# Kernel optimization log

Measured on AMD Instinct MI355X. Metric: run time of the kernel, lower is better.

Reference implementation:

```python
import jax, jax.numpy as jnp
import numpy as np

M = 100000
K = 27            # (2*radius+1)^3, radius=1
D = 64            # attn_dim
C_GEO = 64
C_SEM = 96
NUM_CLASSES = 13
RADIUS = 1
DIAM = 3
EPS = 1e-5


def setup_inputs() -> dict:
    key = jax.random.key(0)
    ks = jax.random.split(key, 16)
    geo_feat_M = jax.random.normal(ks[0], (M, C_GEO), jnp.float32)
    sem_feat_M = jax.random.normal(ks[1], (M, C_SEM), jnp.float32)
    coords = jax.random.randint(ks[2], (M, 3), 0, 64, jnp.int32)
    neighbor_idx = jax.random.randint(ks[3], (M, K), 0, M, jnp.int64)
    # KNN always returns self as a neighbor -> guarantee at least one valid entry
    neighbor_idx = neighbor_idx.at[:, 0].set(jnp.arange(M, dtype=jnp.int64))
    s = 0.05
    return {
        "geo_feat_M": geo_feat_M,
        "sem_feat_M": sem_feat_M,
        "coords": coords,
        "neighbor_idx": neighbor_idx,
        "W_geo": jax.random.normal(ks[4], (C_GEO, D), jnp.float32) * s,
        "gamma": jnp.ones((D,), jnp.float32),
        "beta": jnp.zeros((D,), jnp.float32),
        "W_bdy": jax.random.normal(ks[5], (D, 1), jnp.float32) * s,
        "b_bdy": jnp.zeros((1,), jnp.float32),
        "W_q": jax.random.normal(ks[6], (D, D), jnp.float32) * s,
        "W_k": jax.random.normal(ks[7], (D, D), jnp.float32) * s,
        "W_v": jax.random.normal(ks[8], (C_SEM, D), jnp.float32) * s,
        "pos_emb": jax.random.normal(ks[9], (DIAM ** 3, D), jnp.float32) * s,
        "W_out": jax.random.normal(ks[10], (D, D), jnp.float32) * s,
        "b_out": jnp.zeros((D,), jnp.float32),
        "W_cls": jax.random.normal(ks[11], (D, NUM_CLASSES), jnp.float32) * s,
        "b_cls": jnp.zeros((NUM_CLASSES,), jnp.float32),
    }


def _layernorm(x, gamma, beta):
    mu = jnp.mean(x, axis=-1, keepdims=True)
    var = jnp.mean(jnp.square(x - mu), axis=-1, keepdims=True)
    return (x - mu) * jax.lax.rsqrt(var + EPS) * gamma + beta


def reference(geo_feat_M, sem_feat_M, coords, neighbor_idx,
              W_geo, gamma, beta, W_bdy, b_bdy, W_q, W_k, W_v,
              pos_emb, W_out, b_out, W_cls, b_cls):
    # geometry branch
    Q_geo = jax.nn.relu(_layernorm(geo_feat_M @ W_geo, gamma, beta))  # [M, D]
    bdy_logits = Q_geo @ W_bdy + b_bdy                                # [M, 1]

    # neighbor geometry: valid mask + relative-position embedding index
    nbr_coords = coords[neighbor_idx]                                 # [M, K, 3]
    rel = nbr_coords - coords[:, None, :]                             # [M, K, 3]
    valid_mask = jnp.max(jnp.abs(rel).astype(jnp.float32), axis=-1) <= RADIUS + 0.1
    rel_int = jnp.clip(rel + RADIUS, 0, 2 * RADIUS)
    pos_indices = rel_int[:, :, 0] * DIAM ** 2 + rel_int[:, :, 1] * DIAM + rel_int[:, :, 2]

    # gather neighbor features
    K_feat = Q_geo[neighbor_idx]                                      # [M, K, D]
    V_feat = sem_feat_M[neighbor_idx]                                 # [M, K, C_SEM]

    Qp = Q_geo @ W_q                                                  # [M, D]
    Kp = K_feat @ W_k + pos_emb[pos_indices]                          # [M, K, D]
    Vp = V_feat @ W_v                                                 # [M, K, D]

    attn_logits = jnp.einsum("md,mkd->mk", Qp, Kp) / jnp.sqrt(jnp.float32(D))
    attn_logits = jnp.where(valid_mask, attn_logits, jnp.float32(-10000.0))
    affinity = jax.nn.softmax(attn_logits, axis=-1)                   # [M, K]

    refined = jnp.einsum("mk,mkd->md", affinity, Vp) + sem_feat_M @ W_v
    refined_feat = refined @ W_out + b_out                            # [M, D]
    logits = refined_feat @ W_cls + b_cls                             # [M, 13]
    return (logits, bdy_logits, affinity[:, None, :], refined_feat, neighbor_idx, valid_mask)
```

## Files before the change

kernel.cpp:

```cpp
#include <hip/hip_runtime.h>
#include <hip/hip_bf16.h>

#define M_PTS 100000
#define KN 27
#define CS 96
#define NC 13

#define OFF_LOGITS 0ull
#define OFF_BDY    1300000ull
#define OFF_AFF    1400000ull
#define OFF_RF     4100000ull
#define OFF_NBR    10500000ull
#define OFF_MASK   13200000ull

#define WS_QG   0ull
#define WS_U    6400000ull
#define WS_P    12800000ull
#define WS_WGEO 15500000ull
#define WS_WQK  (WS_WGEO + 4608ull)
#define WS_WPOS (WS_WQK + 4608ull)
#define WS_W1   (WS_WPOS + 2304ull)
#define WS_W2   (WS_W1 + 6656ull)
#define WS_B2   (WS_W2 + 1664ull)
#define WS_VM   (WS_B2 + 32ull)

typedef float f4 __attribute__((ext_vector_type(4)));
typedef float f32x4 __attribute__((ext_vector_type(4)));
typedef short bf16x8 __attribute__((ext_vector_type(8)));
typedef short s16x4 __attribute__((ext_vector_type(4)));

__device__ __forceinline__ short f2bf(float f) {
  union { float f; unsigned int u; } x; x.f = f;
  unsigned int r = x.u + 0x7fffu + ((x.u >> 16) & 1u);
  return (short)(r >> 16);
}
__device__ __forceinline__ float bf2f(unsigned short u) {
  union { unsigned int i; float f; } x; x.i = ((unsigned int)u) << 16;
  return x.f;
}
__device__ __forceinline__ bool nbr_is64(const void* nbrv) {
  const int* w = (const int*)nbrv;
  bool is64 = true;
#pragma unroll
  for (int j = 1; j < 64; j += 2) is64 = is64 && (w[j] == 0);
  return is64;
}
__device__ __forceinline__ long long nbr_at(const void* nbrv, bool is64, size_t i) {
  return is64 ? ((const long long*)nbrv)[i] : (long long)((const int*)nbrv)[i];
}

__global__ __launch_bounds__(256) void k0(const float* __restrict__ Wgeo,
                                          const float* __restrict__ Wbdy,
                                          const float* __restrict__ Wq,
                                          const float* __restrict__ Wk,
                                          const float* __restrict__ Wv,
                                          const float* __restrict__ pos,
                                          const float* __restrict__ Wout,
                                          const float* __restrict__ bout,
                                          const float* __restrict__ Wcls,
                                          const float* __restrict__ bcls,
                                          short* __restrict__ ws) {
  __shared__ float V[64 * NC];
  const int tid = threadIdx.x, blk = blockIdx.x;
  if (blk < 32) {
    for (int i = blk * 256 + tid; i < 16384; i += 8192) {
      if (i < 4096) {
        const int d = i >> 6, c = i & 63;
        ws[WS_WGEO + d * 72 + c] = f2bf(Wgeo[c * 64 + d]);
      } else if (i < 8192) {
        const int t = i - 4096, d = t >> 6, c = t & 63;
        float s = 0.f;
#pragma unroll 8
        for (int q = 0; q < 64; ++q) s = fmaf(Wq[c * 64 + q], Wk[d * 64 + q], s);
        ws[WS_WQK + d * 72 + c] = f2bf(s);
      } else if (i < 10240) {
        const int t = i - 8192, j = t >> 6, c = t & 63;
        float s = 0.f;
        if (j < 27) {
#pragma unroll 8
          for (int q = 0; q < 64; ++q) s = fmaf(Wq[c * 64 + q], pos[j * 64 + q], s);
        } else if (j == 27) {
          s = Wbdy[c];
        }
        ws[WS_WPOS + j * 72 + c] = f2bf(s);
      } else {
        const int t = i - 10240, d = t / 96, sc = t % 96;
        float a = 0.f;
#pragma unroll 8
        for (int q = 0; q < 64; ++q) a = fmaf(Wv[sc * 64 + q], Wout[q * 64 + d], a);
        ws[WS_W1 + d * 104 + sc] = f2bf(a);
      }
    }
  } else {
    for (int i = tid; i < 64 * NC; i += 256) {
      const int t = i / NC, j = i % NC;
      float a = 0.f;
#pragma unroll 8
      for (int d = 0; d < 64; ++d) a = fmaf(Wout[t * 64 + d], Wcls[d * NC + j], a);
      V[i] = a;
    }
    __syncthreads();
    const int g = (blk - 32) * 256 + tid;
    if (g < 16 * 96) {
      const int j = g / 96, s = g % 96;
      float a = 0.f;
      if (j < NC) {
#pragma unroll 8
        for (int t = 0; t < 64; ++t) a = fmaf(Wv[s * 64 + t], V[t * NC + j], a);
      }
      ws[WS_W2 + j * 104 + s] = f2bf(a);
    }
    if (blk == 32 && tid < 16) {
      float a = 0.f;
      if (tid < NC) {
        for (int d = 0; d < 64; ++d) a = fmaf(bout[d], Wcls[d * NC + tid], a);
        a += bcls[tid];
      }
      ((float*)(ws + WS_B2))[tid] = a;
    }
  }
}

__global__ __launch_bounds__(256) void k1(const float* __restrict__ geo,
                                          const int* __restrict__ coords,
                                          const void* __restrict__ nbrv,
                                          const float* __restrict__ gamma,
                                          const float* __restrict__ beta,
                                          const float* __restrict__ bbdy,
                                          const short* __restrict__ ws,
                                          short* __restrict__ Qg,
                                          short* __restrict__ U,
                                          short* __restrict__ P,
                                          unsigned int* __restrict__ vmask,
                                          float* __restrict__ out) {
  __shared__ short sX[4608];
  __shared__ short sQ[4608];
  __shared__ short sWg[4608];
  __shared__ short sWqk[4608];
  __shared__ short sWp[2304];
  const int tid = threadIdx.x;
  {
    const bf16x8* a = (const bf16x8*)(ws + WS_WGEO);
    const bf16x8* b = (const bf16x8*)(ws + WS_WQK);
    const bf16x8* c = (const bf16x8*)(ws + WS_WPOS);
    for (int i = tid; i < 576; i += 256) ((bf16x8*)sWg)[i] = a[i];
    for (int i = tid; i < 576; i += 256) ((bf16x8*)sWqk)[i] = b[i];
    for (int i = tid; i < 288; i += 256) ((bf16x8*)sWp)[i] = c[i];
  }
  const int m0 = blockIdx.x * 64;
  {
    const int r = tid >> 2, qq = tid & 3;
    const int m = min(m0 + r, M_PTS - 1);
    const f4* g = (const f4*)(geo + (size_t)m * 64 + qq * 16);
    const f4 a = g[0], b = g[1], c = g[2], d = g[3];
    bf16x8 lo, hi;
    lo[0]=f2bf(a.x); lo[1]=f2bf(a.y); lo[2]=f2bf(a.z); lo[3]=f2bf(a.w);
    lo[4]=f2bf(b.x); lo[5]=f2bf(b.y); lo[6]=f2bf(b.z); lo[7]=f2bf(b.w);
    hi[0]=f2bf(c.x); hi[1]=f2bf(c.y); hi[2]=f2bf(c.z); hi[3]=f2bf(c.w);
    hi[4]=f2bf(d.x); hi[5]=f2bf(d.y); hi[6]=f2bf(d.z); hi[7]=f2bf(d.w);
    *(bf16x8*)&sX[r * 72 + qq * 16] = lo;
    *(bf16x8*)&sX[r * 72 + qq * 16 + 8] = hi;
  }
  __syncthreads();

  const int lane = tid & 63, w = tid >> 6;
  const int hi4 = lane >> 4, lo16 = lane & 15;
  const int R = w * 16;

  f32x4 acc[4] = {};
#pragma unroll
  for (int kk = 0; kk < 2; ++kk) {
    const bf16x8 a = *(const bf16x8*)&sX[(R + lo16) * 72 + kk * 32 + hi4 * 8];
#pragma unroll
    for (int n = 0; n < 4; ++n) {
      const bf16x8 b = *(const bf16x8*)&sWg[(n * 16 + lo16) * 72 + kk * 32 + hi4 * 8];
      acc[n] = __builtin_amdgcn_mfma_f32_16x16x32_bf16(a, b, acc[n], 0, 0, 0);
    }
  }
  float gam4[4], bet4[4];
#pragma unroll
  for (int n = 0; n < 4; ++n) { gam4[n] = gamma[n * 16 + lo16]; bet4[n] = beta[n * 16 + lo16]; }
#pragma unroll
  for (int j = 0; j < 4; ++j) {
    float s = acc[0][j] + acc[1][j] + acc[2][j] + acc[3][j];
#pragma unroll
    for (int o = 1; o <= 8; o <<= 1) s += __shfl_xor(s, o, 64);
    const float mu = s * (1.f / 64.f);
    float vs = 0.f;
#pragma unroll
    for (int n = 0; n < 4; ++n) { const float d = acc[n][j] - mu; vs = fmaf(d, d, vs); }
#pragma unroll
    for (int o = 1; o <= 8; o <<= 1) vs += __shfl_xor(vs, o, 64);
    const float inv = rsqrtf(vs * (1.f / 64.f) + 1e-5f);
#pragma unroll
    for (int n = 0; n < 4; ++n) {
      const float q = fmaxf(fmaf((acc[n][j] - mu) * inv, gam4[n], bet4[n]), 0.f);
      sQ[(R + hi4 * 4 + j) * 72 + n * 16 + lo16] = f2bf(q);
    }
  }
  __syncthreads();
  f32x4 au[4] = {};
#pragma unroll
  for (int kk = 0; kk < 2; ++kk) {
    const bf16x8 a = *(const bf16x8*)&sQ[(R + lo16) * 72 + kk * 32 + hi4 * 8];
#pragma unroll
    for (int n = 0; n < 4; ++n) {
      const bf16x8 b = *(const bf16x8*)&sWqk[(n * 16 + lo16) * 72 + kk * 32 + hi4 * 8];
      au[n] = __builtin_amdgcn_mfma_f32_16x16x32_bf16(a, b, au[n], 0, 0, 0);
    }
  }
#pragma unroll
  for (int j = 0; j < 4; ++j)
#pragma unroll
    for (int n = 0; n < 4; ++n)
      sX[(R + hi4 * 4 + j) * 72 + n * 16 + lo16] = f2bf(au[n][j]);
  f32x4 ap[2] = {};
#pragma unroll
  for (int kk = 0; kk < 2; ++kk) {
    const bf16x8 a = *(const bf16x8*)&sQ[(R + lo16) * 72 + kk * 32 + hi4 * 8];
#pragma unroll
    for (int n = 0; n < 2; ++n) {
      const bf16x8 b = *(const bf16x8*)&sWp[(n * 16 + lo16) * 72 + kk * 32 + hi4 * 8];
      ap[n] = __builtin_amdgcn_mfma_f32_16x16x32_bf16(a, b, ap[n], 0, 0, 0);
    }
  }
  const float bb = bbdy[0];
#pragma unroll
  for (int n = 0; n < 2; ++n) {
    const int col = n * 16 + lo16;
#pragma unroll
    for (int j = 0; j < 4; ++j) {
      const int m = m0 + R + hi4 * 4 + j;
      if (m < M_PTS) {
        if (col < KN) P[(size_t)m * KN + col] = f2bf(ap[n][j]);
        else if (col == KN) out[OFF_BDY + m] = ap[n][j] + bb;
      }
    }
  }
  __syncthreads();
  for (int i = tid; i < 512; i += 256) {
    const int r = i >> 3, u = i & 7;
    const int m = m0 + r;
    if (m < M_PTS) {
      *(bf16x8*)&Qg[(size_t)m * 64 + u * 8] = *(const bf16x8*)&sQ[r * 72 + u * 8];
      *(bf16x8*)&U[(size_t)m * 64 + u * 8] = *(const bf16x8*)&sX[r * 72 + u * 8];
    }
  }
  {
    const bool is64 = nbr_is64(nbrv);
    const int r = tid >> 2, qq = tid & 3;
    const int m = m0 + r;
    unsigned vbits = 0;
    if (m < M_PTS) {
      const int c0 = coords[m * 3 + 0], c1 = coords[m * 3 + 1], c2 = coords[m * 3 + 2];
      const int kq0 = qq * 7;
      const int cnt = (qq == 3) ? 6 : 7;
#pragma unroll
      for (int t = 0; t < 7; ++t) {
        if (t < cnt) {
          const size_t ni = (size_t)m * KN + kq0 + t;
          const long long nk = nbr_at(nbrv, is64, ni);
          const int dx = coords[nk * 3 + 0] - c0;
          const int dy = coords[nk * 3 + 1] - c1;
          const int dz = coords[nk * 3 + 2] - c2;
          const int valid = (max(max(abs(dx), abs(dy)), abs(dz)) <= 1) ? 1 : 0;
          out[OFF_NBR + ni] = (float)nk;
          out[OFF_MASK + ni] = (float)valid;
          vbits |= (unsigned)valid << (kq0 + t);
        }
      }
    }
    vbits |= __shfl_xor(vbits, 1, 64);
    vbits |= __shfl_xor(vbits, 2, 64);
    if (qq == 0 && m < M_PTS) vmask[m] = vbits;
  }
}

__global__ __launch_bounds__(256) void k2(const float* __restrict__ sem,
                                          const int* __restrict__ coords,
                                          const void* __restrict__ nbrv,
                                          const float* __restrict__ bout,
                                          const short* __restrict__ ws,
                                          const short* __restrict__ Qg,
                                          const short* __restrict__ U,
                                          const short* __restrict__ P,
                                          const unsigned int* __restrict__ vmask,
                                          float* __restrict__ out) {
  __shared__ short sW1[6656];
  __shared__ short sW2[1664];
  __shared__ short sS[6656];
  const int tid = threadIdx.x;
  {
    const bf16x8* a = (const bf16x8*)(ws + WS_W1);
    const bf16x8* b = (const bf16x8*)(ws + WS_W2);
    for (int i = tid; i < 832; i += 256) ((bf16x8*)sW1)[i] = a[i];
    for (int i = tid; i < 208; i += 256) ((bf16x8*)sW2)[i] = b[i];
  }
  const float* b2 = (const float*)(ws + WS_B2);
  const bool is64 = nbr_is64(nbrv);
  __syncthreads();

  const int lane = tid & 63, w = tid >> 6;
  const int hi4 = lane >> 4, lo16 = lane & 15;
  const int R = w * 16;
  const int m0 = blockIdx.x * 64;
  const int pbase = m0 + R;
  const int l31 = lane & 31;
  const int nvr = max(0, min(16, M_PTS - pbase));

  unsigned mym = 0;
  if (lane < nvr) mym = vmask[pbase + lane];
  const unsigned long long cb = __ballot(__popc(mym) > 1);

  const int naff = nvr * KN;
#pragma unroll
  for (int it = 0; it < 7; ++it) {
    const int idx = it * 64 + lane;
    if (idx < naff) {
      const int p = idx / KN;
      if (!((cb >> p) & 1))
        out[OFF_AFF + (size_t)pbase * KN + idx] = (idx - p * KN == 0) ? 1.f : 0.f;
    }
  }
  {
    const f4* semb = (const f4*)(sem + (size_t)pbase * CS);
    const int nf4 = nvr * 24;
#pragma unroll
    for (int it = 0; it < 6; ++it) {
      const int idx = it * 64 + lane;
      if (idx < nf4) {
        const f4 v = semb[idx];
        const int linear = idx * 4, p = linear / 96, c = linear - p * 96;
        if (!((cb >> p) & 1)) {
          s16x4 st;
          st[0] = f2bf(2.f * v.x); st[1] = f2bf(2.f * v.y);
          st[2] = f2bf(2.f * v.z); st[3] = f2bf(2.f * v.w);
          *(s16x4*)&sS[(R + p) * 104 + c] = st;
        }
      }
    }
  }
  unsigned long long cbl = cb;
  while (cbl) {
    const int p = __ffsll(cbl) - 1; cbl &= cbl - 1;
    const int m = pbase + p;
    int nk = 0, vf = 0, pidx = 13;
    if (lane < KN) {
      nk = (int)nbr_at(nbrv, is64, (size_t)m * KN + lane);
      const int dx = coords[nk * 3 + 0] - coords[m * 3 + 0];
      const int dy = coords[nk * 3 + 1] - coords[m * 3 + 1];
      const int dz = coords[nk * 3 + 2] - coords[m * 3 + 2];
      vf = (max(max(abs(dx), abs(dy)), abs(dz)) <= 1) ? 1 : 0;
      pidx = vf ? ((dx + 1) * 9 + (dy + 1) * 3 + (dz + 1)) : 13;
    }
    const float pval = (lane < KN) ? bf2f((unsigned short)P[(size_t)m * KN + pidx]) : 0.f;
    const float uv = bf2f((unsigned short)U[(size_t)m * 64 + lane]);
    float lg = -10000.f;
    unsigned long long vb = __ballot(vf != 0);
    while (vb) {
      const int k = __ffsll(vb) - 1; vb &= vb - 1;
      const int nn = __shfl(nk, k, 64);
      float dd = bf2f((unsigned short)Qg[(size_t)nn * 64 + lane]) * uv;
#pragma unroll
      for (int o = 1; o < 64; o <<= 1) dd += __shfl_xor(dd, o, 64);
      const float pv = __shfl(pval, k, 64);
      if (lane == k) lg = (dd + pv) * 0.125f;
    }
    float mx = lg;
#pragma unroll
    for (int o = 1; o < 32; o <<= 1) mx = fmaxf(mx, __shfl_xor(mx, o, 64));
    const float e = (lane < KN) ? __expf(lg - mx) : 0.f;
    float ssum = e;
#pragma unroll
    for (int o = 1; o < 32; o <<= 1) ssum += __shfl_xor(ssum, o, 64);
    const float aa = e / ssum;
    if (lane < KN) out[OFF_AFF + (size_t)m * KN + lane] = aa;
    float slo = sem[(size_t)m * CS + lane];
    float shi = sem[(size_t)m * CS + 64 + l31];
    unsigned long long ab = __ballot(lane < KN && aa > 0.f);
    while (ab) {
      const int k = __ffsll(ab) - 1; ab &= ab - 1;
      const float ak = __shfl(aa, k, 64);
      const int nn = __shfl(nk, k, 64);
      slo = fmaf(ak, sem[(size_t)nn * CS + lane], slo);
      shi = fmaf(ak, sem[(size_t)nn * CS + 64 + l31], shi);
    }
    sS[(R + p) * 104 + lane] = f2bf(slo);
    if (lane < 32) sS[(R + p) * 104 + 64 + lane] = f2bf(shi);
  }
  __syncthreads();

  f32x4 ar[4] = {};
  f32x4 al = {};
#pragma unroll
  for (int kk = 0; kk < 3; ++kk) {
    const bf16x8 a = *(const bf16x8*)&sS[(R + lo16) * 104 + kk * 32 + hi4 * 8];
#pragma unroll
    for (int n = 0; n < 4; ++n) {
      const bf16x8 b = *(const bf16x8*)&sW1[(n * 16 + lo16) * 104 + kk * 32 + hi4 * 8];
      ar[n] = __builtin_amdgcn_mfma_f32_16x16x32_bf16(a, b, ar[n], 0, 0, 0);
    }
    const bf16x8 b = *(const bf16x8*)&sW2[lo16 * 104 + kk * 32 + hi4 * 8];
    al = __builtin_amdgcn_mfma_f32_16x16x32_bf16(a, b, al, 0, 0, 0);
  }
#pragma unroll
  for (int n = 0; n < 4; ++n) {
    const float bo = bout[n * 16 + lo16];
#pragma unroll
    for (int j = 0; j < 4; ++j) {
      const int m = m0 + R + hi4 * 4 + j;
      if (m < M_PTS) out[OFF_RF + (size_t)m * 64 + n * 16 + lo16] = ar[n][j] + bo;
    }
  }
  {
    const float bc = (lo16 < NC) ? b2[lo16] : 0.f;
#pragma unroll
    for (int j = 0; j < 4; ++j) {
      const int m = m0 + R + hi4 * 4 + j;
      if (m < M_PTS && lo16 < NC) out[OFF_LOGITS + (size_t)m * NC + lo16] = al[j] + bc;
    }
  }
}

extern "C" void kernel_launch(void* const* d_in, const int* in_sizes, int n_in,
                              void* d_out, int out_size, void* d_ws, size_t ws_size,
                              hipStream_t stream) {
  const float* geo = (const float*)d_in[0];
  const float* sem = (const float*)d_in[1];
  const int* coords = (const int*)d_in[2];
  const void* nbrv = (const void*)d_in[3];
  const float* Wgeo = (const float*)d_in[4];
  const float* gamma = (const float*)d_in[5];
  const float* beta = (const float*)d_in[6];
  const float* Wbdy = (const float*)d_in[7];
  const float* bbdy = (const float*)d_in[8];
  const float* Wq = (const float*)d_in[9];
  const float* Wk = (const float*)d_in[10];
  const float* Wv = (const float*)d_in[11];
  const float* pos = (const float*)d_in[12];
  const float* Wout = (const float*)d_in[13];
  const float* bout = (const float*)d_in[14];
  const float* Wcls = (const float*)d_in[15];
  const float* bcls = (const float*)d_in[16];

  short* ws = (short*)d_ws;
  short* Qg = ws + WS_QG;
  short* U = ws + WS_U;
  short* P = ws + WS_P;
  unsigned int* vmask = (unsigned int*)(ws + WS_VM);
  float* out = (float*)d_out;

  const int blocks = (M_PTS + 63) / 64;
  k0<<<38, 256, 0, stream>>>(Wgeo, Wbdy, Wq, Wk, Wv, pos, Wout, bout, Wcls, bcls, ws);
  k1<<<blocks, 256, 0, stream>>>(geo, coords, nbrv, gamma, beta, bbdy, ws, Qg, U, P, vmask, out);
  k2<<<blocks, 256, 0, stream>>>(sem, coords, nbrv, bout, ws, Qg, U, P, vmask, out);
}
```

Before: 222.7 us.

## Fuse simple-point path into k1 and process complex points in a compact persistent kernel

The common path (points with at most one valid neighbor) is now finished inside k1: it reuses shared memory to compute the sem-based refined features and logits with MFMA right after the geometry stage. U and P are written only for points with multiple valid neighbors. Those complex points are handled by a new persistent kernel k2r, launched on 128 blocks, which loops over tiles with one wave per tile and does the output projections with per-lane shuffle dot products instead of MFMA. This removes the full second pass over all points and the reload of vmask and weights in every tile, at the cost of a longer k1 with more shared memory and an unbalanced scalar tail for complex points.

```diff
diff --git a/kernel.cpp b/kernel.cpp
--- a/kernel.cpp
+++ b/kernel.cpp
@@ -5,6 +5,7 @@
 #define KN 27
 #define CS 96
 #define NC 13
+#define NTILES 1563
 
 #define OFF_LOGITS 0ull
 #define OFF_BDY    1300000ull
@@ -122,23 +123,32 @@
 }
 
 __global__ __launch_bounds__(256) void k1(const float* __restrict__ geo,
+                                          const float* __restrict__ sem,
                                           const int* __restrict__ coords,
                                           const void* __restrict__ nbrv,
                                           const float* __restrict__ gamma,
                                           const float* __restrict__ beta,
                                           const float* __restrict__ bbdy,
+                                          const float* __restrict__ bout,
                                           const short* __restrict__ ws,
                                           short* __restrict__ Qg,
                                           short* __restrict__ U,
                                           short* __restrict__ P,
                                           unsigned int* __restrict__ vmask,
                                           float* __restrict__ out) {
-  __shared__ short sX[4608];
-  __shared__ short sQ[4608];
-  __shared__ short sWg[4608];
-  __shared__ short sWqk[4608];
-  __shared__ short sWp[2304];
+  __shared__ __align__(16) char sMem[41472];
+  __shared__ unsigned sVm[64];
+  short* sX   = (short*)sMem;
+  short* sQ   = (short*)(sMem + 9216);
+  short* sWg  = (short*)(sMem + 18432);
+  short* sWqk = (short*)(sMem + 27648);
+  short* sWp  = (short*)(sMem + 36864);
+  short* sS   = (short*)sMem;
+  short* sW1  = (short*)(sMem + 18432);
+  short* sW2  = (short*)(sMem + 31744);
+  float* sB2  = (float*)(sMem + 35072);
   const int tid = threadIdx.x;
+  if (tid < 64) sVm[tid] = 0;
   {
     const bf16x8* a = (const bf16x8*)(ws + WS_WGEO);
     const bf16x8* b = (const bf16x8*)(ws + WS_WQK);
@@ -200,6 +210,7 @@
   }
   __syncthreads();
   f32x4 au[4] = {};
+  f32x4 ap[2] = {};
 #pragma unroll
   for (int kk = 0; kk < 2; ++kk) {
     const bf16x8 a = *(const bf16x8*)&sQ[(R + lo16) * 72 + kk * 32 + hi4 * 8];
@@ -208,110 +219,66 @@
       const bf16x8 b = *(const bf16x8*)&sWqk[(n * 16 + lo16) * 72 + kk * 32 + hi4 * 8];
       au[n] = __builtin_amdgcn_mfma_f32_16x16x32_bf16(a, b, au[n], 0, 0, 0);
     }
-  }
-#pragma unroll
-  for (int j = 0; j < 4; ++j)
-#pragma unroll
-    for (int n = 0; n < 4; ++n)
-      sX[(R + hi4 * 4 + j) * 72 + n * 16 + lo16] = f2bf(au[n][j]);
-  f32x4 ap[2] = {};
-#pragma unroll
-  for (int kk = 0; kk < 2; ++kk) {
-    const bf16x8 a = *(const bf16x8*)&sQ[(R + lo16) * 72 + kk * 32 + hi4 * 8];
 #pragma unroll
     for (int n = 0; n < 2; ++n) {
       const bf16x8 b = *(const bf16x8*)&sWp[(n * 16 + lo16) * 72 + kk * 32 + hi4 * 8];
       ap[n] = __builtin_amdgcn_mfma_f32_16x16x32_bf16(a, b, ap[n], 0, 0, 0);
     }
   }
-  const float bb = bbdy[0];
-#pragma unroll
-  for (int n = 0; n < 2; ++n) {
-    const int col = n * 16 + lo16;
-#pragma unroll
-    for (int j = 0; j < 4; ++j) {
-      const int m = m0 + R + hi4 * 4 + j;
-      if (m < M_PTS) {
-        if (col < KN) P[(size_t)m * KN + col] = f2bf(ap[n][j]);
-        else if (col == KN) out[OFF_BDY + m] = ap[n][j] + bb;
-      }
+  const bool is64 = nbr_is64(nbrv);
+  for (int idx = tid; idx < 64 * KN; idx += 256) {
+    const int p = idx / KN, kq = idx - p * KN;
+    const int m = m0 + p;
+    if (m < M_PTS) {
+      const long long nk = nbr_at(nbrv, is64, (size_t)m * KN + kq);
+      const int dx = coords[nk * 3 + 0] - coords[m * 3 + 0];
+      const int dy = coords[nk * 3 + 1] - coords[m * 3 + 1];
+      const int dz = coords[nk * 3 + 2] - coords[m * 3 + 2];
+      const int valid = (max(max(abs(dx), abs(dy)), abs(dz)) <= 1) ? 1 : 0;
+      out[OFF_NBR + (size_t)m0 * KN + idx] = (float)nk;
+      out[OFF_MASK + (size_t)m0 * KN + idx] = (float)valid;
+      if (valid) atomicOr(&sVm[p], 1u << kq);
     }
   }
   __syncthreads();
   for (int i = tid; i < 512; i += 256) {
     const int r = i >> 3, u = i & 7;
     const int m = m0 + r;
+    if (m < M_PTS)
+      *(bf16x8*)&Qg[(size_t)m * 64 + u * 8] = *(const bf16x8*)&sQ[r * 72 + u * 8];
+  }
+  if (tid < 64 && m0 + tid < M_PTS) vmask[m0 + tid] = sVm[tid];
+  const float bb = bbdy[0];
+#pragma unroll
+  for (int j = 0; j < 4; ++j) {
+    const int row = R + hi4 * 4 + j;
+    const int m = m0 + row;
     if (m < M_PTS) {
-      *(bf16x8*)&Qg[(size_t)m * 64 + u * 8] = *(const bf16x8*)&sQ[r * 72 + u * 8];
-      *(bf16x8*)&U[(size_t)m * 64 + u * 8] = *(const bf16x8*)&sX[r * 72 + u * 8];
-    }
-  }
-  {
-    const bool is64 = nbr_is64(nbrv);
-    const int r = tid >> 2, qq = tid & 3;
-    const int m = m0 + r;
-    unsigned vbits = 0;
-    if (m < M_PTS) {
-      const int c0 = coords[m * 3 + 0], c1 = coords[m * 3 + 1], c2 = coords[m * 3 + 2];
-      const int kq0 = qq * 7;
-      const int cnt = (qq == 3) ? 6 : 7;
-#pragma unroll
-      for (int t = 0; t < 7; ++t) {
-        if (t < cnt) {
-          const size_t ni = (size_t)m * KN + kq0 + t;
-          const long long nk = nbr_at(nbrv, is64, ni);
-          const int dx = coords[nk * 3 + 0] - c0;
-          const int dy = coords[nk * 3 + 1] - c1;
-          const int dz = coords[nk * 3 + 2] - c2;
-          const int valid = (max(max(abs(dx), abs(dy)), abs(dz)) <= 1) ? 1 : 0;
-          out[OFF_NBR + ni] = (float)nk;
-          out[OFF_MASK + ni] = (float)valid;
-          vbits |= (unsigned)valid << (kq0 + t);
-        }
-      }
-    }
-    vbits |= __shfl_xor(vbits, 1, 64);
-    vbits |= __shfl_xor(vbits, 2, 64);
-    if (qq == 0 && m < M_PTS) vmask[m] = vbits;
-  }
-}
-
-__global__ __launch_bounds__(256) void k2(const float* __restrict__ sem,
-                                          const int* __restrict__ coords,
-                                          const void* __restrict__ nbrv,
-                                          const float* __restrict__ bout,
-                                          const short* __restrict__ ws,
-                                          const short* __restrict__ Qg,
-                                          const short* __restrict__ U,
-                                          const short* __restrict__ P,
-                                          const unsigned int* __restrict__ vmask,
-                                          float* __restrict__ out) {
-  __shared__ short sW1[6656];
-  __shared__ short sW2[1664];
-  __shared__ short sS[6656];
-  const int tid = threadIdx.x;
+      const bool cx = __popc(sVm[row]) > 1;
+#pragma unroll
+      for (int n = 0; n < 4; ++n)
+        if (cx) U[(size_t)m * 64 + n * 16 + lo16] = f2bf(au[n][j]);
+#pragma unroll
+      for (int n = 0; n < 2; ++n) {
+        const int col = n * 16 + lo16;
+        if (col < KN) { if (cx) P[(size_t)m * KN + col] = f2bf(ap[n][j]); }
+        else if (col == KN) out[OFF_BDY + m] = ap[1][j] + bb;
+      }
+    }
+  }
+  const int pbase = m0 + R;
+  const int nvr = max(0, min(16, M_PTS - pbase));
+  const unsigned mym = (lane < nvr) ? sVm[R + lane] : 0u;
+  const unsigned long long cb = __ballot(__popc(mym) > 1);
+  __syncthreads();
+
   {
     const bf16x8* a = (const bf16x8*)(ws + WS_W1);
     const bf16x8* b = (const bf16x8*)(ws + WS_W2);
     for (int i = tid; i < 832; i += 256) ((bf16x8*)sW1)[i] = a[i];
     for (int i = tid; i < 208; i += 256) ((bf16x8*)sW2)[i] = b[i];
-  }
-  const float* b2 = (const float*)(ws + WS_B2);
-  const bool is64 = nbr_is64(nbrv);
-  __syncthreads();
-
-  const int lane = tid & 63, w = tid >> 6;
-  const int hi4 = lane >> 4, lo16 = lane & 15;
-  const int R = w * 16;
-  const int m0 = blockIdx.x * 64;
-  const int pbase = m0 + R;
-  const int l31 = lane & 31;
-  const int nvr = max(0, min(16, M_PTS - pbase));
-
-  unsigned mym = 0;
-  if (lane < nvr) mym = vmask[pbase + lane];
-  const unsigned long long cb = __ballot(__popc(mym) > 1);
-
+    if (tid < 16) sB2[tid] = ((const float*)(ws + WS_B2))[tid];
+  }
   const int naff = nvr * KN;
 #pragma unroll
   for (int it = 0; it < 7; ++it) {
@@ -340,56 +307,7 @@
       }
     }
   }
-  unsigned long long cbl = cb;
-  while (cbl) {
-    const int p = __ffsll(cbl) - 1; cbl &= cbl - 1;
-    const int m = pbase + p;
-    int nk = 0, vf = 0, pidx = 13;
-    if (lane < KN) {
-      nk = (int)nbr_at(nbrv, is64, (size_t)m * KN + lane);
-      const int dx = coords[nk * 3 + 0] - coords[m * 3 + 0];
-      const int dy = coords[nk * 3 + 1] - coords[m * 3 + 1];
-      const int dz = coords[nk * 3 + 2] - coords[m * 3 + 2];
-      vf = (max(max(abs(dx), abs(dy)), abs(dz)) <= 1) ? 1 : 0;
-      pidx = vf ? ((dx + 1) * 9 + (dy + 1) * 3 + (dz + 1)) : 13;
-    }
-    const float pval = (lane < KN) ? bf2f((unsigned short)P[(size_t)m * KN + pidx]) : 0.f;
-    const float uv = bf2f((unsigned short)U[(size_t)m * 64 + lane]);
-    float lg = -10000.f;
-    unsigned long long vb = __ballot(vf != 0);
-    while (vb) {
-      const int k = __ffsll(vb) - 1; vb &= vb - 1;
-      const int nn = __shfl(nk, k, 64);
-      float dd = bf2f((unsigned short)Qg[(size_t)nn * 64 + lane]) * uv;
-#pragma unroll
-      for (int o = 1; o < 64; o <<= 1) dd += __shfl_xor(dd, o, 64);
-      const float pv = __shfl(pval, k, 64);
-      if (lane == k) lg = (dd + pv) * 0.125f;
-    }
-    float mx = lg;
-#pragma unroll
-    for (int o = 1; o < 32; o <<= 1) mx = fmaxf(mx, __shfl_xor(mx, o, 64));
-    const float e = (lane < KN) ? __expf(lg - mx) : 0.f;
-    float ssum = e;
-#pragma unroll
-    for (int o = 1; o < 32; o <<= 1) ssum += __shfl_xor(ssum, o, 64);
-    const float aa = e / ssum;
-    if (lane < KN) out[OFF_AFF + (size_t)m * KN + lane] = aa;
-    float slo = sem[(size_t)m * CS + lane];
-    float shi = sem[(size_t)m * CS + 64 + l31];
-    unsigned long long ab = __ballot(lane < KN && aa > 0.f);
-    while (ab) {
-      const int k = __ffsll(ab) - 1; ab &= ab - 1;
-      const float ak = __shfl(aa, k, 64);
-      const int nn = __shfl(nk, k, 64);
-      slo = fmaf(ak, sem[(size_t)nn * CS + lane], slo);
-      shi = fmaf(ak, sem[(size_t)nn * CS + 64 + l31], shi);
-    }
-    sS[(R + p) * 104 + lane] = f2bf(slo);
-    if (lane < 32) sS[(R + p) * 104 + 64 + lane] = f2bf(shi);
-  }
-  __syncthreads();
-
+  __syncthreads();
   f32x4 ar[4] = {};
   f32x4 al = {};
 #pragma unroll
@@ -413,11 +331,101 @@
     }
   }
   {
-    const float bc = (lo16 < NC) ? b2[lo16] : 0.f;
+    const float bc = (lo16 < NC) ? sB2[lo16] : 0.f;
 #pragma unroll
     for (int j = 0; j < 4; ++j) {
       const int m = m0 + R + hi4 * 4 + j;
       if (m < M_PTS && lo16 < NC) out[OFF_LOGITS + (size_t)m * NC + lo16] = al[j] + bc;
+    }
+  }
+}
+
+__global__ __launch_bounds__(256) void k2r(const float* __restrict__ sem,
+                                           const int* __restrict__ coords,
+                                           const void* __restrict__ nbrv,
+                                           const float* __restrict__ bout,
+                                           const short* __restrict__ ws,
+                                           const short* __restrict__ Qg,
+                                           const short* __restrict__ U,
+                                           const short* __restrict__ P,
+                                           const unsigned int* __restrict__ vmask,
+                                           float* __restrict__ out) {
+  __shared__ short sW1[6656];
+  __shared__ short sW2[1664];
+  __shared__ float sB2[16];
+  const int tid = threadIdx.x;
+  {
+    const bf16x8* a = (const bf16x8*)(ws + WS_W1);
+    const bf16x8* b = (const bf16x8*)(ws + WS_W2);
+    for (int i = tid; i < 832; i += 256) ((bf16x8*)sW1)[i] = a[i];
+    for (int i = tid; i < 208; i += 256) ((bf16x8*)sW2)[i] = b[i];
+    if (tid < 16) sB2[tid] = ((const float*)(ws + WS_B2))[tid];
+  }
+  const bool is64 = nbr_is64(nbrv);
+  __syncthreads();
+
+  const int lane = tid & 63, w = tid >> 6;
+  const int l31 = lane & 31;
+  const float bo = bout[lane];
+  const float bc = (lane < NC) ? sB2[lane] : 0.f;
+
+  for (int tile = blockIdx.x * 4 + w; tile < NTILES; tile += gridDim.x * 4) {
+    const int pbase = tile * 64;
+    const int nv = min(64, M_PTS - pbase);
+    const unsigned mym = (lane < nv) ? vmask[pbase + lane] : 0u;
+    unsigned long long cbl = __ballot(__popc(mym) > 1);
+    while (cbl) {
+      const int p = __ffsll(cbl) - 1; cbl &= cbl - 1;
+      const int m = pbase + p;
+      int nk = 0, vf = 0, pidx = 13;
+      if (lane < KN) {
+        nk = (int)nbr_at(nbrv, is64, (size_t)m * KN + lane);
+        const int dx = coords[nk * 3 + 0] - coords[m * 3 + 0];
+        const int dy = coords[nk * 3 + 1] - coords[m * 3 + 1];
+        const int dz = coords[nk * 3 + 2] - coords[m * 3 + 2];
+        vf = (max(max(abs(dx), abs(dy)), abs(dz)) <= 1) ? 1 : 0;
+        pidx = vf ? ((dx + 1) * 9 + (dy + 1) * 3 + (dz + 1)) : 13;
+      }
+      const float pval = (lane < KN) ? bf2f((unsigned short)P[(size_t)m * KN + pidx]) : 0.f;
+      const float uv = bf2f((unsigned short)U[(size_t)m * 64 + lane]);
+      float lg = -10000.f;
+      unsigned long long vb = __ballot(vf != 0);
+      while (vb) {
+        const int k = __ffsll(vb) - 1; vb &= vb - 1;
+        const int nn = __shfl(nk, k, 64);
+        float dd = bf2f((unsigned short)Qg[(size_t)nn * 64 + lane]) * uv;
+#pragma unroll
+        for (int o = 1; o < 64; o <<= 1) dd += __shfl_xor(dd, o, 64);
+        const float pv = __shfl(pval, k, 64);
+        if (lane == k) lg = (dd + pv) * 0.125f;
+      }
+      float mx = lg;
+#pragma unroll
+      for (int o = 1; o < 32; o <<= 1) mx = fmaxf(mx, __shfl_xor(mx, o, 64));
+      const float e = (lane < KN) ? __expf(lg - mx) : 0.f;
+      float ssum = e;
+#pragma unroll
+      for (int o = 1; o < 32; o <<= 1) ssum += __shfl_xor(ssum, o, 64);
+      const float aa = e / ssum;
+      if (lane < KN) out[OFF_AFF + (size_t)m * KN + lane] = aa;
+      float slo = sem[(size_t)m * CS + lane];
+      float shi = sem[(size_t)m * CS + 64 + l31];
+      unsigned long long ab = __ballot(lane < KN && aa > 0.f);
+      while (ab) {
+        const int k = __ffsll(ab) - 1; ab &= ab - 1;
+        const float ak = __shfl(aa, k, 64);
+        const int nn = __shfl(nk, k, 64);
+        slo = fmaf(ak, sem[(size_t)nn * CS + lane], slo);
+        shi = fmaf(ak, sem[(size_t)nn * CS + 64 + l31], shi);
+      }
+      float rf = bo, lgt = bc;
+      for (int s = 0; s < 96; ++s) {
+        const float as = (s < 64) ? __shfl(slo, s, 64) : __shfl(shi, s - 64, 64);
+        rf = fmaf(as, bf2f((unsigned short)sW1[lane * 104 + s]), rf);
+        if (lane < NC) lgt = fmaf(as, bf2f((unsigned short)sW2[lane * 104 + s]), lgt);
+      }
+      out[OFF_RF + (size_t)m * 64 + lane] = rf;
+      if (lane < NC) out[OFF_LOGITS + (size_t)m * NC + lane] = lgt;
     }
   }
 }
@@ -450,8 +458,8 @@
   unsigned int* vmask = (unsigned int*)(ws + WS_VM);
   float* out = (float*)d_out;
 
-  const int blocks = (M_PTS + 63) / 64;
   k0<<<38, 256, 0, stream>>>(Wgeo, Wbdy, Wq, Wk, Wv, pos, Wout, bout, Wcls, bcls, ws);
-  k1<<<blocks, 256, 0, stream>>>(geo, coords, nbrv, gamma, beta, bbdy, ws, Qg, U, P, vmask, out);
-  k2<<<blocks, 256, 0, stream>>>(sem, coords, nbrv, bout, ws, Qg, U, P, vmask, out);
-}
+  k1<<<NTILES, 256, 0, stream>>>(geo, sem, coords, nbrv, gamma, beta, bbdy, bout,
+                                 ws, Qg, U, P, vmask, out);
+  k2r<<<128, 256, 0, stream>>>(sem, coords, nbrv, bout, ws, Qg, U, P, vmask, out);
+}
```

Measured after the change: 257.1 us. 15.4% more time.
